# Kernel optimization log

Measured on AMD Instinct MI355X. Metric: run time of the kernel, lower is better.

Reference implementation:

```python
import jax, jax.numpy as jnp
import numpy as np

K = 7          # involution kernel size
PAD = (K - 1) // 2
C = 256        # channels
GC = 16        # group_channels (hardcoded in module)
G = C // GC    # groups = 16
RED = C // 4   # reduction channels = 64
EPS = 1e-5


def _bn_eval(x, gamma, beta, mean, var):
    # eval-mode BatchNorm2d over channel dim of NCHW
    inv = gamma / jnp.sqrt(var + EPS)
    return x * inv[None, :, None, None] + (beta - mean * inv)[None, :, None, None]


def setup_inputs() -> dict:
    key = jax.random.key(0)
    ks = jax.random.split(key, 12)
    x = jax.random.normal(ks[0], (8, C, 56, 56), dtype=jnp.float32)
    # conv1: 1x1, C -> C/4, no bias (followed by BN+ReLU)
    w1 = jax.random.normal(ks[1], (RED, C), dtype=jnp.float32) * (1.0 / np.sqrt(C))
    bn1_gamma = 1.0 + 0.1 * jax.random.normal(ks[2], (RED,), dtype=jnp.float32)
    bn1_beta = 0.1 * jax.random.normal(ks[3], (RED,), dtype=jnp.float32)
    bn1_mean = 0.1 * jax.random.normal(ks[4], (RED,), dtype=jnp.float32)
    bn1_var = jax.random.uniform(ks[5], (RED,), dtype=jnp.float32, minval=0.5, maxval=1.5)
    # conv2: 1x1, C/4 -> K^2 * groups, with bias, no BN/act
    w2 = jax.random.normal(ks[6], (K * K * G, RED), dtype=jnp.float32) * (1.0 / np.sqrt(RED))
    b2 = 0.1 * jax.random.normal(ks[7], (K * K * G,), dtype=jnp.float32)
    # final BN on output channels
    bn2_gamma = 1.0 + 0.1 * jax.random.normal(ks[8], (C,), dtype=jnp.float32)
    bn2_beta = 0.1 * jax.random.normal(ks[9], (C,), dtype=jnp.float32)
    bn2_mean = 0.1 * jax.random.normal(ks[10], (C,), dtype=jnp.float32)
    bn2_var = jax.random.uniform(ks[11], (C,), dtype=jnp.float32, minval=0.5, maxval=1.5)
    return {
        "x": x, "w1": w1,
        "bn1_gamma": bn1_gamma, "bn1_beta": bn1_beta, "bn1_mean": bn1_mean, "bn1_var": bn1_var,
        "w2": w2, "b2": b2,
        "bn2_gamma": bn2_gamma, "bn2_beta": bn2_beta, "bn2_mean": bn2_mean, "bn2_var": bn2_var,
    }


def reference(x, w1, bn1_gamma, bn1_beta, bn1_mean, bn1_var,
              w2, b2, bn2_gamma, bn2_beta, bn2_mean, bn2_var):
    b, c, h, w = x.shape
    # --- kernel generation branch (stride == 1, no avgpool) ---
    t = jnp.einsum('bchw,oc->bohw', x, w1)            # [b, RED, h, w]
    t = jax.nn.relu(_bn_eval(t, bn1_gamma, bn1_beta, bn1_mean, bn1_var))
    wgt = jnp.einsum('bchw,oc->bohw', t, w2) + b2[None, :, None, None]  # [b, K^2*G, h, w]
    wgt = wgt.reshape(b, G, K * K, h, w)
    # --- unfold: patches ordered (c, kh, kw) to match nn.Unfold ---
    xp = jnp.pad(x, ((0, 0), (0, 0), (PAD, PAD), (PAD, PAD)))
    patches = jnp.stack(
        [xp[:, :, i:i + h, j:j + w] for i in range(K) for j in range(K)],
        axis=2,
    )  # [b, c, K^2, h, w]
    patches = patches.reshape(b, G, GC, K * K, h, w)
    # --- per-pixel multiply-sum over kernel footprint ---
    out = jnp.einsum('bgkhw,bgckhw->bgchw', wgt, patches).reshape(b, c, h, w)
    out = jax.nn.relu(_bn_eval(out, bn2_gamma, bn2_beta, bn2_mean, bn2_var))
    return out
```

## Files before the change

kernel.cpp:

```cpp
#include <hip/hip_runtime.h>
#include <hip/hip_fp16.h>

#define NB   8
#define NC   256
#define HW   56
#define NPX  3136
#define RED  64
#define NG   16
#define GC   16
#define KS   7
#define KK   49
#define PADK 3
#define XPH  62
#define XPW  64
#define XPSLICE (XPH * XPW)
#define XT_RS 72
#define XT_CS 584
#define WSTR  68

typedef float f32x4 __attribute__((ext_vector_type(4)));
typedef _Float16 h16x4 __attribute__((ext_vector_type(4)));
typedef _Float16 h16x8 __attribute__((ext_vector_type(8)));

__global__ __launch_bounds__(256) void prep_kernel(
    const float* __restrict__ x, const float* __restrict__ w1,
    const float* __restrict__ w2, _Float16* __restrict__ xpad,
    _Float16* __restrict__ w1h, _Float16* __restrict__ w2h) {
    int bid = blockIdx.x;
    if (bid < NB * NC) {
        const float* xs = x + (size_t)bid * NPX;
        _Float16* xd = xpad + (size_t)bid * XPSLICE;
#pragma unroll 4
        for (int e = threadIdx.x; e < XPSLICE; e += 256) {
            int row = e >> 6, col = e & 63;
            int h = row - PADK, w = col - PADK;
            float v = (h >= 0 && h < HW && w >= 0 && w < HW) ? xs[h * HW + w] : 0.0f;
            xd[e] = (_Float16)v;
        }
    } else if (bid < NB * NC + NG) {
        int g = bid - NB * NC;
#pragma unroll 4
        for (int e = threadIdx.x; e < 4096; e += 256) {
            int m = e >> 6, k = e & 63;
            float v = (m < KK) ? w2[((size_t)g * KK + m) * RED + k] : 0.0f;
            w2h[(size_t)g * 4096 + e] = (_Float16)v;
        }
    } else {
#pragma unroll 4
        for (int e = threadIdx.x; e < 64 * 256; e += 256)
            w1h[e] = (_Float16)w1[e];
    }
}

__global__ __launch_bounds__(64) void conv1_kernel(
    const _Float16* __restrict__ xpad, const _Float16* __restrict__ w1h,
    const float* __restrict__ g1, const float* __restrict__ be1,
    const float* __restrict__ mu1, const float* __restrict__ var1,
    _Float16* __restrict__ tT) {
    int lane = threadIdx.x;
    int l15 = lane & 15, l4 = lane >> 4;
    int wgid = blockIdx.x;
    int b  = wgid & 7;
    int nt = wgid >> 3;
    int px = nt * 16 + l15;
    int h = px / HW, w = px % HW;

    const _Float16* xp = xpad + (size_t)b * NC * XPSLICE
                       + (h + PADK) * XPW + (w + PADK);

    f32x4 acc0 = {0,0,0,0}, acc1 = {0,0,0,0}, acc2 = {0,0,0,0}, acc3 = {0,0,0,0};
#pragma unroll
    for (int kk = 0; kk < 8; ++kk) {
        h16x8 bfr;
#pragma unroll
        for (int i = 0; i < 8; ++i)
            bfr[i] = xp[(size_t)(kk * 32 + l4 * 8 + i) * XPSLICE];
#pragma unroll
        for (int mt = 0; mt < 4; ++mt) {
            const _Float16* ap = w1h + (mt * 16 + l15) * NC + kk * 32 + l4 * 8;
            h16x8 a = *(const h16x8*)ap;
            f32x4 c = (mt == 0) ? acc0 : (mt == 1) ? acc1 : (mt == 2) ? acc2 : acc3;
            c = __builtin_amdgcn_mfma_f32_16x16x32_f16(a, bfr, c, 0, 0, 0);
            if (mt == 0) acc0 = c; else if (mt == 1) acc1 = c;
            else if (mt == 2) acc2 = c; else acc3 = c;
        }
    }

    _Float16* tb = tT + ((size_t)b * NPX + px) * RED;
#pragma unroll
    for (int mt = 0; mt < 4; ++mt) {
        f32x4 a = (mt == 0) ? acc0 : (mt == 1) ? acc1 : (mt == 2) ? acc2 : acc3;
        int o0 = mt * 16 + l4 * 4;
        h16x4 pk;
#pragma unroll
        for (int r = 0; r < 4; ++r) {
            int o = o0 + r;
            float inv = g1[o] * rsqrtf(var1[o] + 1e-5f);
            float v = a[r] * inv + (be1[o] - mu1[o] * inv);
            pk[r] = (_Float16)fmaxf(v, 0.0f);
        }
        *(h16x4*)(tb + o0) = pk;
    }
}

__global__ __launch_bounds__(256, 5) void involution_kernel(
    const _Float16* __restrict__ xpad, const _Float16* __restrict__ tT,
    const _Float16* __restrict__ w2h, const float* __restrict__ b2,
    const float* __restrict__ g2, const float* __restrict__ be2,
    const float* __restrict__ mu2, const float* __restrict__ var2,
    float* __restrict__ out) {
    __shared__ __align__(16) _Float16 xtap[GC * XT_CS];
    __shared__ __align__(16) _Float16 wls[KK * WSTR];

    int tid  = threadIdx.x;
    int lane = tid & 63;
    int wv   = __builtin_amdgcn_readfirstlane(tid >> 6);
    int wgid = blockIdx.x;
    int swz  = (wgid & 7) * 784 + (wgid >> 3);
    int tile = swz % 49;
    int g    = (swz / 49) & 15;
    int b    = swz / 784;
    int px0 = tile * 64;
    int h0  = px0 / HW;

    const _Float16* xpg = xpad + ((size_t)b * NC + (size_t)g * GC) * XPSLICE;

    h16x8 xr[4];
#pragma unroll
    for (int u = 0; u < 4; ++u) {
        int cid = u * 256 + tid;
        int ch  = cid >> 6;
        int rem = cid & 63;
        int rr  = rem >> 3, c8 = rem & 7;
        xr[u] = *(const h16x8*)(xpg + (size_t)ch * XPSLICE + (h0 + rr) * XPW + c8 * 8);
    }

    {
        int l15 = lane & 15, l4 = lane >> 4;
        int pxc = px0 + wv * 16 + l15;
        const _Float16* tp = tT + ((size_t)b * NPX + pxc) * RED + l4 * 8;
        h16x8 bfr0 = *(const h16x8*)tp;
        h16x8 bfr1 = *(const h16x8*)(tp + 32);

        const _Float16* wA = w2h + (size_t)g * 4096;
        const float* bg = b2 + (size_t)g * KK;
        f32x4 acc0 = {0,0,0,0}, acc1 = {0,0,0,0}, acc2 = {0,0,0,0}, acc3 = {0,0,0,0};
#pragma unroll
        for (int mt = 0; mt < 4; ++mt) {
            const _Float16* ap = wA + (mt * 16 + l15) * 64 + l4 * 8;
            h16x8 a0 = *(const h16x8*)(ap);
            h16x8 a1 = *(const h16x8*)(ap + 32);
            f32x4 a = (mt == 0) ? acc0 : (mt == 1) ? acc1 : (mt == 2) ? acc2 : acc3;
            a = __builtin_amdgcn_mfma_f32_16x16x32_f16(a0, bfr0, a, 0, 0, 0);
            a = __builtin_amdgcn_mfma_f32_16x16x32_f16(a1, bfr1, a, 0, 0, 0);
            if (mt == 0) acc0 = a; else if (mt == 1) acc1 = a;
            else if (mt == 2) acc2 = a; else acc3 = a;
        }
        _Float16* wl = wls + wv * 16 + l15;
#pragma unroll
        for (int mt = 0; mt < 4; ++mt) {
            f32x4 a = (mt == 0) ? acc0 : (mt == 1) ? acc1 : (mt == 2) ? acc2 : acc3;
#pragma unroll
            for (int r = 0; r < 4; ++r) {
                int k = mt * 16 + l4 * 4 + r;
                if (k < KK) wl[k * WSTR] = (_Float16)(a[r] + bg[k]);
            }
        }
    }

#pragma unroll
    for (int u = 0; u < 4; ++u) {
        int cid = u * 256 + tid;
        int ch  = cid >> 6;
        int rem = cid & 63;
        int rr  = rem >> 3, c8 = rem & 7;
        *(h16x8*)&xtap[ch * XT_CS + rr * XT_RS + c8 * 8] = xr[u];
    }
    __syncthreads();

    int quad = tid & 15;
    int ch   = tid >> 4;
    int pxl  = quad * 4;
    int px_a = px0 + pxl;
    int lh   = px_a / HW - h0;
    int w0   = px_a % HW;

    const _Float16* xr0 = xtap + ch * XT_CS + lh * XT_RS + w0;
    float acc0 = 0.f, acc1 = 0.f, acc2 = 0.f, acc3 = 0.f;
#pragma unroll
    for (int i = 0; i < KS; ++i) {
        h16x4 t0 = *(const h16x4*)(xr0 + i * XT_RS);
        h16x4 t1 = *(const h16x4*)(xr0 + i * XT_RS + 4);
        h16x4 t2 = *(const h16x4*)(xr0 + i * XT_RS + 8);
        float cc[12];
        cc[0] = (float)t0[0]; cc[1]  = (float)t0[1]; cc[2]  = (float)t0[2]; cc[3]  = (float)t0[3];
        cc[4] = (float)t1[0]; cc[5]  = (float)t1[1]; cc[6]  = (float)t1[2]; cc[7]  = (float)t1[3];
        cc[8] = (float)t2[0]; cc[9]  = (float)t2[1]; cc[10] = (float)t2[2]; cc[11] = (float)t2[3];
#pragma unroll
        for (int j = 0; j < KS; ++j) {
            h16x4 wp = *(const h16x4*)&wls[(i * KS + j) * WSTR + pxl];
            acc0 = fmaf((float)wp[0], cc[j + 0], acc0);
            acc1 = fmaf((float)wp[1], cc[j + 1], acc1);
            acc2 = fmaf((float)wp[2], cc[j + 2], acc2);
            acc3 = fmaf((float)wp[3], cc[j + 3], acc3);
        }
    }

    int c_ = g * GC + ch;
    float inv = g2[c_] * rsqrtf(var2[c_] + 1e-5f);
    float off = be2[c_] - mu2[c_] * inv;
    f32x4 o;
    o[0] = fmaxf(acc0 * inv + off, 0.0f);
    o[1] = fmaxf(acc1 * inv + off, 0.0f);
    o[2] = fmaxf(acc2 * inv + off, 0.0f);
    o[3] = fmaxf(acc3 * inv + off, 0.0f);
    *(f32x4*)(out + ((size_t)b * NC + c_) * NPX + px_a) = o;
}

extern "C" void kernel_launch(void* const* d_in, const int* in_sizes, int n_in,
                              void* d_out, int out_size, void* d_ws, size_t ws_size,
                              hipStream_t stream) {
    const float* x    = (const float*)d_in[0];
    const float* w1   = (const float*)d_in[1];
    const float* g1   = (const float*)d_in[2];
    const float* be1  = (const float*)d_in[3];
    const float* mu1  = (const float*)d_in[4];
    const float* var1 = (const float*)d_in[5];
    const float* w2   = (const float*)d_in[6];
    const float* b2   = (const float*)d_in[7];
    const float* g2   = (const float*)d_in[8];
    const float* be2  = (const float*)d_in[9];
    const float* mu2  = (const float*)d_in[10];
    const float* var2 = (const float*)d_in[11];
    float* outp = (float*)d_out;

    _Float16* xpad = (_Float16*)d_ws;
    char* p = (char*)d_ws + (size_t)NB * NC * XPSLICE * sizeof(_Float16);
    _Float16* tT = (_Float16*)p;
    p += (size_t)NB * NPX * RED * sizeof(_Float16);
    _Float16* w2h = (_Float16*)p;
    p += (size_t)NG * 4096 * sizeof(_Float16);
    _Float16* w1h = (_Float16*)p;

    prep_kernel<<<NB * NC + NG + 1, 256, 0, stream>>>(x, w1, w2, xpad, w1h, w2h);
    conv1_kernel<<<1568, 64, 0, stream>>>(xpad, w1h, g1, be1, mu1, var1, tT);
    involution_kernel<<<6272, 256, 0, stream>>>(
        xpad, tT, w2h, b2, g2, be2, mu2, var2, outp);
}
```

Before: 64.70 us.

## Add pixel-major fp16 copy of x so conv1 reads contiguous channel vectors

```diff
diff --git a/kernel.cpp b/kernel.cpp
--- a/kernel.cpp
+++ b/kernel.cpp
@@ -25,85 +25,104 @@
 __global__ __launch_bounds__(256) void prep_kernel(
     const float* __restrict__ x, const float* __restrict__ w1,
     const float* __restrict__ w2, _Float16* __restrict__ xpad,
-    _Float16* __restrict__ w1h, _Float16* __restrict__ w2h) {
+    _Float16* __restrict__ xT, _Float16* __restrict__ w1h,
+    _Float16* __restrict__ w2h) {
     int bid = blockIdx.x;
-    if (bid < NB * NC) {
-        const float* xs = x + (size_t)bid * NPX;
-        _Float16* xd = xpad + (size_t)bid * XPSLICE;
-#pragma unroll 4
-        for (int e = threadIdx.x; e < XPSLICE; e += 256) {
-            int row = e >> 6, col = e & 63;
-            int h = row - PADK, w = col - PADK;
-            float v = (h >= 0 && h < HW && w >= 0 && w < HW) ? xs[h * HW + w] : 0.0f;
-            xd[e] = (_Float16)v;
-        }
-    } else if (bid < NB * NC + NG) {
-        int g = bid - NB * NC;
+    if (bid < 392) {
+        __shared__ _Float16 tls[64][65];
+        int b = bid & 7, tile = bid >> 3;
+        int px0 = tile * 64;
+        int lane = threadIdx.x & 63;
+        int cq = threadIdx.x >> 6;
+        int px = px0 + lane;
+        int h = px / HW, w = px % HW;
+        const float* xb = x + (size_t)b * NC * NPX;
+#pragma unroll 1
+        for (int pass = 0; pass < 4; ++pass) {
+#pragma unroll
+            for (int rd = 0; rd < 16; ++rd) {
+                int c = pass * 64 + rd * 4 + cq;
+                _Float16 hv = (_Float16)xb[(size_t)c * NPX + px];
+                xpad[((size_t)b * NC + c) * XPSLICE + (h + PADK) * XPW + (w + PADK)] = hv;
+                tls[rd * 4 + cq][lane] = hv;
+            }
+            __syncthreads();
+#pragma unroll
+            for (int rd = 0; rd < 16; ++rd) {
+                int pxw = rd * 4 + cq;
+                xT[((size_t)b * NPX + px0 + pxw) * NC + pass * 64 + lane] =
+                    tls[lane][pxw];
+            }
+            __syncthreads();
+        }
+    } else if (bid < 408) {
+        int g = bid - 392;
 #pragma unroll 4
         for (int e = threadIdx.x; e < 4096; e += 256) {
             int m = e >> 6, k = e & 63;
             float v = (m < KK) ? w2[((size_t)g * KK + m) * RED + k] : 0.0f;
             w2h[(size_t)g * 4096 + e] = (_Float16)v;
         }
-    } else {
+    } else if (bid == 408) {
 #pragma unroll 4
         for (int e = threadIdx.x; e < 64 * 256; e += 256)
             w1h[e] = (_Float16)w1[e];
-    }
-}
-
-__global__ __launch_bounds__(64) void conv1_kernel(
-    const _Float16* __restrict__ xpad, const _Float16* __restrict__ w1h,
+    } else {
+        int blk = bid - 409;
+        int b = blk & 7;
+        int c0 = (blk >> 3) * 8;
+#pragma unroll 1
+        for (int si = 0; si < 8; ++si) {
+            _Float16* xd = xpad + ((size_t)b * NC + c0 + si) * XPSLICE;
+            for (int e = threadIdx.x; e < 832; e += 256) {
+                int row, col;
+                if (e < 192)      { row = e >> 6;              col = e & 63; }
+                else if (e < 384) { int f = e - 192; row = 59 + (f >> 6); col = f & 63; }
+                else              { int f = e - 384; row = 3 + (f >> 3);
+                                    int c8 = f & 7;  col = (c8 < 3) ? c8 : 56 + c8; }
+                xd[row * XPW + col] = (_Float16)0.0f;
+            }
+        }
+    }
+}
+
+__global__ __launch_bounds__(256) void conv1_kernel(
+    const _Float16* __restrict__ xT, const _Float16* __restrict__ w1h,
     const float* __restrict__ g1, const float* __restrict__ be1,
     const float* __restrict__ mu1, const float* __restrict__ var1,
     _Float16* __restrict__ tT) {
-    int lane = threadIdx.x;
-    int l15 = lane & 15, l4 = lane >> 4;
+    int lane = threadIdx.x & 63;
+    int wv   = __builtin_amdgcn_readfirstlane(threadIdx.x >> 6);
     int wgid = blockIdx.x;
     int b  = wgid & 7;
     int nt = wgid >> 3;
+    int l15 = lane & 15, l4 = lane >> 4;
     int px = nt * 16 + l15;
-    int h = px / HW, w = px % HW;
-
-    const _Float16* xp = xpad + (size_t)b * NC * XPSLICE
-                       + (h + PADK) * XPW + (w + PADK);
-
-    f32x4 acc0 = {0,0,0,0}, acc1 = {0,0,0,0}, acc2 = {0,0,0,0}, acc3 = {0,0,0,0};
+
+    const _Float16* bp = xT + ((size_t)b * NPX + px) * NC + l4 * 8;
+    const _Float16* ap = w1h + (wv * 16 + l15) * NC + l4 * 8;
+
+    f32x4 acc = {0, 0, 0, 0};
 #pragma unroll
     for (int kk = 0; kk < 8; ++kk) {
-        h16x8 bfr;
-#pragma unroll
-        for (int i = 0; i < 8; ++i)
-            bfr[i] = xp[(size_t)(kk * 32 + l4 * 8 + i) * XPSLICE];
-#pragma unroll
-        for (int mt = 0; mt < 4; ++mt) {
-            const _Float16* ap = w1h + (mt * 16 + l15) * NC + kk * 32 + l4 * 8;
-            h16x8 a = *(const h16x8*)ap;
-            f32x4 c = (mt == 0) ? acc0 : (mt == 1) ? acc1 : (mt == 2) ? acc2 : acc3;
-            c = __builtin_amdgcn_mfma_f32_16x16x32_f16(a, bfr, c, 0, 0, 0);
-            if (mt == 0) acc0 = c; else if (mt == 1) acc1 = c;
-            else if (mt == 2) acc2 = c; else acc3 = c;
-        }
-    }
-
-    _Float16* tb = tT + ((size_t)b * NPX + px) * RED;
-#pragma unroll
-    for (int mt = 0; mt < 4; ++mt) {
-        f32x4 a = (mt == 0) ? acc0 : (mt == 1) ? acc1 : (mt == 2) ? acc2 : acc3;
-        int o0 = mt * 16 + l4 * 4;
-        h16x4 pk;
-#pragma unroll
-        for (int r = 0; r < 4; ++r) {
-            int o = o0 + r;
-            float inv = g1[o] * rsqrtf(var1[o] + 1e-5f);
-            float v = a[r] * inv + (be1[o] - mu1[o] * inv);
-            pk[r] = (_Float16)fmaxf(v, 0.0f);
-        }
-        *(h16x4*)(tb + o0) = pk;
-    }
-}
-
-__global__ __launch_bounds__(256, 5) void involution_kernel(
+        h16x8 bfr = *(const h16x8*)(bp + kk * 32);
+        h16x8 a   = *(const h16x8*)(ap + kk * 32);
+        acc = __builtin_amdgcn_mfma_f32_16x16x32_f16(a, bfr, acc, 0, 0, 0);
+    }
+
+    int o0 = wv * 16 + l4 * 4;
+    h16x4 pk;
+#pragma unroll
+    for (int r = 0; r < 4; ++r) {
+        int o = o0 + r;
+        float inv = g1[o] * rsqrtf(var1[o] + 1e-5f);
+        float v = acc[r] * inv + (be1[o] - mu1[o] * inv);
+        pk[r] = (_Float16)fmaxf(v, 0.0f);
+    }
+    *(h16x4*)(tT + ((size_t)b * NPX + px) * RED + o0) = pk;
+}
+
+__global__ __launch_bounds__(256, 6) void involution_kernel(
     const _Float16* __restrict__ xpad, const _Float16* __restrict__ tT,
     const _Float16* __restrict__ w2h, const float* __restrict__ b2,
     const float* __restrict__ g2, const float* __restrict__ be2,
@@ -235,15 +254,13 @@
     float* outp = (float*)d_out;
 
     _Float16* xpad = (_Float16*)d_ws;
-    char* p = (char*)d_ws + (size_t)NB * NC * XPSLICE * sizeof(_Float16);
-    _Float16* tT = (_Float16*)p;
-    p += (size_t)NB * NPX * RED * sizeof(_Float16);
-    _Float16* w2h = (_Float16*)p;
-    p += (size_t)NG * 4096 * sizeof(_Float16);
-    _Float16* w1h = (_Float16*)p;
-
-    prep_kernel<<<NB * NC + NG + 1, 256, 0, stream>>>(x, w1, w2, xpad, w1h, w2h);
-    conv1_kernel<<<1568, 64, 0, stream>>>(xpad, w1h, g1, be1, mu1, var1, tT);
+    _Float16* xT   = xpad + (size_t)NB * NC * XPSLICE;
+    _Float16* tT   = xT + (size_t)NB * NPX * NC;
+    _Float16* w2h  = tT + (size_t)NB * NPX * RED;
+    _Float16* w1h  = w2h + (size_t)NG * 4096;
+
+    prep_kernel<<<665, 256, 0, stream>>>(x, w1, w2, xpad, xT, w1h, w2h);
+    conv1_kernel<<<1568, 256, 0, stream>>>(xT, w1h, g1, be1, mu1, var1, tT);
     involution_kernel<<<6272, 256, 0, stream>>>(
         xpad, tT, w2h, b2, g2, be2, mu2, var2, outp);
 }
```

After: 71.92 us. 11.2% more time.

## Enlarge involution tile to 4 rows per block with 8 pixels per thread

Applied to the files above, without the earlier changes.

```diff
diff --git a/kernel.cpp b/kernel.cpp
--- a/kernel.cpp
+++ b/kernel.cpp
@@ -14,9 +14,10 @@
 #define XPH  62
 #define XPW  64
 #define XPSLICE (XPH * XPW)
-#define XT_RS 72
-#define XT_CS 584
-#define WSTR  68
+#define TPX  224
+#define NT2  14
+#define XT2_CS 644
+#define WSTR2  232
 
 typedef float f32x4 __attribute__((ext_vector_type(4)));
 typedef _Float16 h16x4 __attribute__((ext_vector_type(4)));
@@ -103,118 +104,137 @@
     }
 }
 
-__global__ __launch_bounds__(256, 5) void involution_kernel(
+__global__ __launch_bounds__(448, 3) void involution_kernel(
     const _Float16* __restrict__ xpad, const _Float16* __restrict__ tT,
     const _Float16* __restrict__ w2h, const float* __restrict__ b2,
     const float* __restrict__ g2, const float* __restrict__ be2,
     const float* __restrict__ mu2, const float* __restrict__ var2,
     float* __restrict__ out) {
-    __shared__ __align__(16) _Float16 xtap[GC * XT_CS];
-    __shared__ __align__(16) _Float16 wls[KK * WSTR];
+    __shared__ __align__(16) _Float16 xtap[GC * XT2_CS];
+    __shared__ __align__(16) _Float16 wls[KK * WSTR2];
 
     int tid  = threadIdx.x;
     int lane = tid & 63;
     int wv   = __builtin_amdgcn_readfirstlane(tid >> 6);
     int wgid = blockIdx.x;
-    int swz  = (wgid & 7) * 784 + (wgid >> 3);
-    int tile = swz % 49;
-    int g    = (swz / 49) & 15;
-    int b    = swz / 784;
-    int px0 = tile * 64;
-    int h0  = px0 / HW;
+    int swz  = (wgid & 7) * 224 + (wgid >> 3);
+    int b    = swz / 224;
+    int rem  = swz % 224;
+    int g    = rem / NT2;
+    int tile = rem % NT2;
+    int px0 = tile * TPX;
+    int R0  = tile * 4;
 
     const _Float16* xpg = xpad + ((size_t)b * NC + (size_t)g * GC) * XPSLICE;
 
-    h16x8 xr[4];
-#pragma unroll
-    for (int u = 0; u < 4; ++u) {
-        int cid = u * 256 + tid;
-        int ch  = cid >> 6;
-        int rem = cid & 63;
-        int rr  = rem >> 3, c8 = rem & 7;
-        xr[u] = *(const h16x8*)(xpg + (size_t)ch * XPSLICE + (h0 + rr) * XPW + c8 * 8);
+    h16x8 xr[3];
+#pragma unroll
+    for (int u = 0; u < 3; ++u) {
+        int cid = u * 448 + tid;
+        if (cid < 1280) {
+            int ch = cid / 80;
+            int rm = cid % 80;
+            int rr = rm >> 3, c8 = rm & 7;
+            xr[u] = *(const h16x8*)(xpg + (size_t)ch * XPSLICE
+                                    + (R0 + rr) * XPW + c8 * 8);
+        }
     }
 
     {
         int l15 = lane & 15, l4 = lane >> 4;
-        int pxc = px0 + wv * 16 + l15;
-        const _Float16* tp = tT + ((size_t)b * NPX + pxc) * RED + l4 * 8;
-        h16x8 bfr0 = *(const h16x8*)tp;
-        h16x8 bfr1 = *(const h16x8*)(tp + 32);
-
         const _Float16* wA = w2h + (size_t)g * 4096;
         const float* bg = b2 + (size_t)g * KK;
-        f32x4 acc0 = {0,0,0,0}, acc1 = {0,0,0,0}, acc2 = {0,0,0,0}, acc3 = {0,0,0,0};
+        h16x8 a0[4], a1[4];
 #pragma unroll
         for (int mt = 0; mt < 4; ++mt) {
             const _Float16* ap = wA + (mt * 16 + l15) * 64 + l4 * 8;
-            h16x8 a0 = *(const h16x8*)(ap);
-            h16x8 a1 = *(const h16x8*)(ap + 32);
-            f32x4 a = (mt == 0) ? acc0 : (mt == 1) ? acc1 : (mt == 2) ? acc2 : acc3;
-            a = __builtin_amdgcn_mfma_f32_16x16x32_f16(a0, bfr0, a, 0, 0, 0);
-            a = __builtin_amdgcn_mfma_f32_16x16x32_f16(a1, bfr1, a, 0, 0, 0);
-            if (mt == 0) acc0 = a; else if (mt == 1) acc1 = a;
-            else if (mt == 2) acc2 = a; else acc3 = a;
-        }
-        _Float16* wl = wls + wv * 16 + l15;
-#pragma unroll
-        for (int mt = 0; mt < 4; ++mt) {
-            f32x4 a = (mt == 0) ? acc0 : (mt == 1) ? acc1 : (mt == 2) ? acc2 : acc3;
-#pragma unroll
-            for (int r = 0; r < 4; ++r) {
-                int k = mt * 16 + l4 * 4 + r;
-                if (k < KK) wl[k * WSTR] = (_Float16)(a[r] + bg[k]);
+            a0[mt] = *(const h16x8*)(ap);
+            a1[mt] = *(const h16x8*)(ap + 32);
+        }
+#pragma unroll
+        for (int it = 0; it < 2; ++it) {
+            int nt = wv * 2 + it;
+            int pxc = px0 + nt * 16 + l15;
+            const _Float16* tp = tT + ((size_t)b * NPX + pxc) * RED + l4 * 8;
+            h16x8 bfr0 = *(const h16x8*)tp;
+            h16x8 bfr1 = *(const h16x8*)(tp + 32);
+
+            f32x4 acc0 = {0,0,0,0}, acc1 = {0,0,0,0},
+                  acc2 = {0,0,0,0}, acc3 = {0,0,0,0};
+#pragma unroll
+            for (int mt = 0; mt < 4; ++mt) {
+                f32x4 a = (mt == 0) ? acc0 : (mt == 1) ? acc1
+                        : (mt == 2) ? acc2 : acc3;
+                a = __builtin_amdgcn_mfma_f32_16x16x32_f16(a0[mt], bfr0, a, 0, 0, 0);
+                a = __builtin_amdgcn_mfma_f32_16x16x32_f16(a1[mt], bfr1, a, 0, 0, 0);
+                if (mt == 0) acc0 = a; else if (mt == 1) acc1 = a;
+                else if (mt == 2) acc2 = a; else acc3 = a;
             }
-        }
-    }
-
-#pragma unroll
-    for (int u = 0; u < 4; ++u) {
-        int cid = u * 256 + tid;
-        int ch  = cid >> 6;
-        int rem = cid & 63;
-        int rr  = rem >> 3, c8 = rem & 7;
-        *(h16x8*)&xtap[ch * XT_CS + rr * XT_RS + c8 * 8] = xr[u];
+            _Float16* wl = wls + nt * 16 + l15;
+#pragma unroll
+            for (int mt = 0; mt < 4; ++mt) {
+                f32x4 a = (mt == 0) ? acc0 : (mt == 1) ? acc1
+                        : (mt == 2) ? acc2 : acc3;
+#pragma unroll
+                for (int r = 0; r < 4; ++r) {
+                    int k = mt * 16 + l4 * 4 + r;
+                    if (k < KK) wl[k * WSTR2] = (_Float16)(a[r] + bg[k]);
+                }
+            }
+        }
+    }
+
+#pragma unroll
+    for (int u = 0; u < 3; ++u) {
+        int cid = u * 448 + tid;
+        if (cid < 1280) {
+            int ch = cid / 80;
+            int rm = cid % 80;
+            int rr = rm >> 3, c8 = rm & 7;
+            *(h16x8*)&xtap[ch * XT2_CS + rr * 64 + c8 * 8] = xr[u];
+        }
     }
     __syncthreads();
 
-    int quad = tid & 15;
-    int ch   = tid >> 4;
-    int pxl  = quad * 4;
-    int px_a = px0 + pxl;
-    int lh   = px_a / HW - h0;
-    int w0   = px_a % HW;
-
-    const _Float16* xr0 = xtap + ch * XT_CS + lh * XT_RS + w0;
-    float acc0 = 0.f, acc1 = 0.f, acc2 = 0.f, acc3 = 0.f;
+    int octet = tid >> 4;
+    int ch    = tid & 15;
+    int lin   = octet * 8;
+    int lh    = lin / 56;
+    int w0    = lin % 56;
+
+    const _Float16* xb0 = xtap + ch * XT2_CS + lh * 64 + w0;
+    float acc[8];
+#pragma unroll
+    for (int p = 0; p < 8; ++p) acc[p] = 0.0f;
+
 #pragma unroll
     for (int i = 0; i < KS; ++i) {
-        h16x4 t0 = *(const h16x4*)(xr0 + i * XT_RS);
-        h16x4 t1 = *(const h16x4*)(xr0 + i * XT_RS + 4);
-        h16x4 t2 = *(const h16x4*)(xr0 + i * XT_RS + 8);
-        float cc[12];
-        cc[0] = (float)t0[0]; cc[1]  = (float)t0[1]; cc[2]  = (float)t0[2]; cc[3]  = (float)t0[3];
-        cc[4] = (float)t1[0]; cc[5]  = (float)t1[1]; cc[6]  = (float)t1[2]; cc[7]  = (float)t1[3];
-        cc[8] = (float)t2[0]; cc[9]  = (float)t2[1]; cc[10] = (float)t2[2]; cc[11] = (float)t2[3];
+        h16x8 t0 = *(const h16x8*)(xb0 + i * 64);
+        h16x8 t1 = *(const h16x8*)(xb0 + i * 64 + 8);
+        float cc[16];
+#pragma unroll
+        for (int p = 0; p < 8; ++p) { cc[p] = (float)t0[p]; cc[8 + p] = (float)t1[p]; }
 #pragma unroll
         for (int j = 0; j < KS; ++j) {
-            h16x4 wp = *(const h16x4*)&wls[(i * KS + j) * WSTR + pxl];
-            acc0 = fmaf((float)wp[0], cc[j + 0], acc0);
-            acc1 = fmaf((float)wp[1], cc[j + 1], acc1);
-            acc2 = fmaf((float)wp[2], cc[j + 2], acc2);
-            acc3 = fmaf((float)wp[3], cc[j + 3], acc3);
+            h16x8 wq = *(const h16x8*)&wls[(i * KS + j) * WSTR2 + lin];
+#pragma unroll
+            for (int p = 0; p < 8; ++p)
+                acc[p] = fmaf((float)wq[p], cc[j + p], acc[p]);
         }
     }
 
     int c_ = g * GC + ch;
     float inv = g2[c_] * rsqrtf(var2[c_] + 1e-5f);
     float off = be2[c_] - mu2[c_] * inv;
-    f32x4 o;
-    o[0] = fmaxf(acc0 * inv + off, 0.0f);
-    o[1] = fmaxf(acc1 * inv + off, 0.0f);
-    o[2] = fmaxf(acc2 * inv + off, 0.0f);
-    o[3] = fmaxf(acc3 * inv + off, 0.0f);
-    *(f32x4*)(out + ((size_t)b * NC + c_) * NPX + px_a) = o;
+    float* op = out + ((size_t)b * NC + c_) * NPX + px0 + lin;
+    f32x4 o0, o1;
+#pragma unroll
+    for (int p = 0; p < 4; ++p) {
+        o0[p] = fmaxf(acc[p] * inv + off, 0.0f);
+        o1[p] = fmaxf(acc[4 + p] * inv + off, 0.0f);
+    }
+    *(f32x4*)(op)     = o0;
+    *(f32x4*)(op + 4) = o1;
 }
 
 extern "C" void kernel_launch(void* const* d_in, const int* in_sizes, int n_in,
@@ -235,15 +255,12 @@
     float* outp = (float*)d_out;
 
     _Float16* xpad = (_Float16*)d_ws;
-    char* p = (char*)d_ws + (size_t)NB * NC * XPSLICE * sizeof(_Float16);
-    _Float16* tT = (_Float16*)p;
-    p += (size_t)NB * NPX * RED * sizeof(_Float16);
-    _Float16* w2h = (_Float16*)p;
-    p += (size_t)NG * 4096 * sizeof(_Float16);
-    _Float16* w1h = (_Float16*)p;
+    _Float16* tT   = xpad + (size_t)NB * NC * XPSLICE;
+    _Float16* w2h  = tT + (size_t)NB * NPX * RED;
+    _Float16* w1h  = w2h + (size_t)NG * 4096;
 
     prep_kernel<<<NB * NC + NG + 1, 256, 0, stream>>>(x, w1, w2, xpad, w1h, w2h);
     conv1_kernel<<<1568, 64, 0, stream>>>(xpad, w1h, g1, be1, mu1, var1, tT);
-    involution_kernel<<<6272, 256, 0, stream>>>(
+    involution_kernel<<<1792, 448, 0, stream>>>(
         xpad, tT, w2h, b2, g2, be2, mu2, var2, outp);
 }
```

After: 64.14 us. No clear change (-0.9%).

## Make involution blocks persistent over four tiles with register double-buffered prefetch

Applied to the files above, without the earlier changes.

```diff
diff --git a/kernel.cpp b/kernel.cpp
--- a/kernel.cpp
+++ b/kernel.cpp
@@ -103,10 +103,10 @@
     }
 }
 
-__global__ __launch_bounds__(256, 5) void involution_kernel(
+__global__ __launch_bounds__(256) void involution_kernel(
     const _Float16* __restrict__ xpad, const _Float16* __restrict__ tT,
     const _Float16* __restrict__ w2h, const float* __restrict__ b2,
-    const float* __restrict__ g2, const float* __restrict__ be2,
+    const float* __restrict__ g2v, const float* __restrict__ be2,
     const float* __restrict__ mu2, const float* __restrict__ var2,
     float* __restrict__ out) {
     __shared__ __align__(16) _Float16 xtap[GC * XT_CS];
@@ -115,106 +115,142 @@
     int tid  = threadIdx.x;
     int lane = tid & 63;
     int wv   = __builtin_amdgcn_readfirstlane(tid >> 6);
-    int wgid = blockIdx.x;
-    int swz  = (wgid & 7) * 784 + (wgid >> 3);
-    int tile = swz % 49;
-    int g    = (swz / 49) & 15;
-    int b    = swz / 784;
-    int px0 = tile * 64;
-    int h0  = px0 / HW;
-
-    const _Float16* xpg = xpad + ((size_t)b * NC + (size_t)g * GC) * XPSLICE;
-
-    h16x8 xr[4];
-#pragma unroll
-    for (int u = 0; u < 4; ++u) {
-        int cid = u * 256 + tid;
-        int ch  = cid >> 6;
-        int rem = cid & 63;
-        int rr  = rem >> 3, c8 = rem & 7;
-        xr[u] = *(const h16x8*)(xpg + (size_t)ch * XPSLICE + (h0 + rr) * XPW + c8 * 8);
-    }
+    int l15 = lane & 15, l4 = lane >> 4;
+    int quad = tid & 15;
+    int chB  = tid >> 4;
+    int bid = blockIdx.x;
+    int b   = bid & 7;
+    int idx = bid >> 3;
+
+    h16x8 xrP[2][4];
+    h16x8 bfP[2][2];
 
     {
-        int l15 = lane & 15, l4 = lane >> 4;
+        int un = idx * 4;
+        int g = un / 49, tile = un % 49;
+        int px0 = tile * 64, h0 = px0 / HW;
+        const _Float16* xpg = xpad + ((size_t)b * NC + (size_t)g * GC) * XPSLICE;
+#pragma unroll
+        for (int su = 0; su < 4; ++su) {
+            int c_ = su * 256 + tid;
+            int ch = c_ >> 6, rem = c_ & 63, rr = rem >> 3, c8 = rem & 7;
+            xrP[0][su] = *(const h16x8*)(xpg + (size_t)ch * XPSLICE
+                                         + (h0 + rr) * XPW + c8 * 8);
+        }
         int pxc = px0 + wv * 16 + l15;
         const _Float16* tp = tT + ((size_t)b * NPX + pxc) * RED + l4 * 8;
-        h16x8 bfr0 = *(const h16x8*)tp;
-        h16x8 bfr1 = *(const h16x8*)(tp + 32);
-
-        const _Float16* wA = w2h + (size_t)g * 4096;
-        const float* bg = b2 + (size_t)g * KK;
-        f32x4 acc0 = {0,0,0,0}, acc1 = {0,0,0,0}, acc2 = {0,0,0,0}, acc3 = {0,0,0,0};
-#pragma unroll
-        for (int mt = 0; mt < 4; ++mt) {
-            const _Float16* ap = wA + (mt * 16 + l15) * 64 + l4 * 8;
-            h16x8 a0 = *(const h16x8*)(ap);
-            h16x8 a1 = *(const h16x8*)(ap + 32);
-            f32x4 a = (mt == 0) ? acc0 : (mt == 1) ? acc1 : (mt == 2) ? acc2 : acc3;
-            a = __builtin_amdgcn_mfma_f32_16x16x32_f16(a0, bfr0, a, 0, 0, 0);
-            a = __builtin_amdgcn_mfma_f32_16x16x32_f16(a1, bfr1, a, 0, 0, 0);
-            if (mt == 0) acc0 = a; else if (mt == 1) acc1 = a;
-            else if (mt == 2) acc2 = a; else acc3 = a;
-        }
-        _Float16* wl = wls + wv * 16 + l15;
-#pragma unroll
-        for (int mt = 0; mt < 4; ++mt) {
-            f32x4 a = (mt == 0) ? acc0 : (mt == 1) ? acc1 : (mt == 2) ? acc2 : acc3;
-#pragma unroll
-            for (int r = 0; r < 4; ++r) {
-                int k = mt * 16 + l4 * 4 + r;
-                if (k < KK) wl[k * WSTR] = (_Float16)(a[r] + bg[k]);
-            }
-        }
+        bfP[0][0] = *(const h16x8*)tp;
+        bfP[0][1] = *(const h16x8*)(tp + 32);
     }
 
 #pragma unroll
     for (int u = 0; u < 4; ++u) {
-        int cid = u * 256 + tid;
-        int ch  = cid >> 6;
-        int rem = cid & 63;
-        int rr  = rem >> 3, c8 = rem & 7;
-        *(h16x8*)&xtap[ch * XT_CS + rr * XT_RS + c8 * 8] = xr[u];
-    }
-    __syncthreads();
-
-    int quad = tid & 15;
-    int ch   = tid >> 4;
-    int pxl  = quad * 4;
-    int px_a = px0 + pxl;
-    int lh   = px_a / HW - h0;
-    int w0   = px_a % HW;
-
-    const _Float16* xr0 = xtap + ch * XT_CS + lh * XT_RS + w0;
-    float acc0 = 0.f, acc1 = 0.f, acc2 = 0.f, acc3 = 0.f;
-#pragma unroll
-    for (int i = 0; i < KS; ++i) {
-        h16x4 t0 = *(const h16x4*)(xr0 + i * XT_RS);
-        h16x4 t1 = *(const h16x4*)(xr0 + i * XT_RS + 4);
-        h16x4 t2 = *(const h16x4*)(xr0 + i * XT_RS + 8);
-        float cc[12];
-        cc[0] = (float)t0[0]; cc[1]  = (float)t0[1]; cc[2]  = (float)t0[2]; cc[3]  = (float)t0[3];
-        cc[4] = (float)t1[0]; cc[5]  = (float)t1[1]; cc[6]  = (float)t1[2]; cc[7]  = (float)t1[3];
-        cc[8] = (float)t2[0]; cc[9]  = (float)t2[1]; cc[10] = (float)t2[2]; cc[11] = (float)t2[3];
-#pragma unroll
-        for (int j = 0; j < KS; ++j) {
-            h16x4 wp = *(const h16x4*)&wls[(i * KS + j) * WSTR + pxl];
-            acc0 = fmaf((float)wp[0], cc[j + 0], acc0);
-            acc1 = fmaf((float)wp[1], cc[j + 1], acc1);
-            acc2 = fmaf((float)wp[2], cc[j + 2], acc2);
-            acc3 = fmaf((float)wp[3], cc[j + 3], acc3);
-        }
-    }
-
-    int c_ = g * GC + ch;
-    float inv = g2[c_] * rsqrtf(var2[c_] + 1e-5f);
-    float off = be2[c_] - mu2[c_] * inv;
-    f32x4 o;
-    o[0] = fmaxf(acc0 * inv + off, 0.0f);
-    o[1] = fmaxf(acc1 * inv + off, 0.0f);
-    o[2] = fmaxf(acc2 * inv + off, 0.0f);
-    o[3] = fmaxf(acc3 * inv + off, 0.0f);
-    *(f32x4*)(out + ((size_t)b * NC + c_) * NPX + px_a) = o;
+        const int cur = u & 1;
+        const int nxt = cur ^ 1;
+        int un = idx * 4 + u;
+        int g = un / 49, tile = un % 49;
+        int px0 = tile * 64, h0 = px0 / HW;
+
+        asm volatile("s_waitcnt lgkmcnt(0)" ::: "memory");
+        __builtin_amdgcn_s_barrier();
+        __builtin_amdgcn_sched_barrier(0);
+
+#pragma unroll
+        for (int su = 0; su < 4; ++su) {
+            int c_ = su * 256 + tid;
+            int ch = c_ >> 6, rem = c_ & 63, rr = rem >> 3, c8 = rem & 7;
+            *(h16x8*)&xtap[ch * XT_CS + rr * XT_RS + c8 * 8] = xrP[cur][su];
+        }
+
+        {
+            const _Float16* wA = w2h + (size_t)g * 4096;
+            const float* bg = b2 + (size_t)g * KK;
+            f32x4 acc0 = {0,0,0,0}, acc1 = {0,0,0,0},
+                  acc2 = {0,0,0,0}, acc3 = {0,0,0,0};
+#pragma unroll
+            for (int mt = 0; mt < 4; ++mt) {
+                const _Float16* ap = wA + (mt * 16 + l15) * 64 + l4 * 8;
+                h16x8 a0 = *(const h16x8*)(ap);
+                h16x8 a1 = *(const h16x8*)(ap + 32);
+                f32x4 a = (mt == 0) ? acc0 : (mt == 1) ? acc1
+                        : (mt == 2) ? acc2 : acc3;
+                a = __builtin_amdgcn_mfma_f32_16x16x32_f16(a0, bfP[cur][0], a, 0, 0, 0);
+                a = __builtin_amdgcn_mfma_f32_16x16x32_f16(a1, bfP[cur][1], a, 0, 0, 0);
+                if (mt == 0) acc0 = a; else if (mt == 1) acc1 = a;
+                else if (mt == 2) acc2 = a; else acc3 = a;
+            }
+            _Float16* wl = wls + wv * 16 + l15;
+#pragma unroll
+            for (int mt = 0; mt < 4; ++mt) {
+                f32x4 a = (mt == 0) ? acc0 : (mt == 1) ? acc1
+                        : (mt == 2) ? acc2 : acc3;
+#pragma unroll
+                for (int r = 0; r < 4; ++r) {
+                    int k = mt * 16 + l4 * 4 + r;
+                    if (k < KK) wl[k * WSTR] = (_Float16)(a[r] + bg[k]);
+                }
+            }
+        }
+
+        int c_out = g * GC + chB;
+        float inv = g2v[c_out] * rsqrtf(var2[c_out] + 1e-5f);
+        float off = be2[c_out] - mu2[c_out] * inv;
+
+        if (u < 3) {
+            int un2 = un + 1;
+            int gN = un2 / 49, tileN = un2 % 49;
+            int px0N = tileN * 64, h0N = px0N / HW;
+            const _Float16* xpgN = xpad + ((size_t)b * NC + (size_t)gN * GC) * XPSLICE;
+#pragma unroll
+            for (int su = 0; su < 4; ++su) {
+                int c_ = su * 256 + tid;
+                int ch = c_ >> 6, rem = c_ & 63, rr = rem >> 3, c8 = rem & 7;
+                xrP[nxt][su] = *(const h16x8*)(xpgN + (size_t)ch * XPSLICE
+                                               + (h0N + rr) * XPW + c8 * 8);
+            }
+            int pxcN = px0N + wv * 16 + l15;
+            const _Float16* tpN = tT + ((size_t)b * NPX + pxcN) * RED + l4 * 8;
+            bfP[nxt][0] = *(const h16x8*)tpN;
+            bfP[nxt][1] = *(const h16x8*)(tpN + 32);
+        }
+
+        asm volatile("s_waitcnt lgkmcnt(0)" ::: "memory");
+        __builtin_amdgcn_s_barrier();
+        __builtin_amdgcn_sched_barrier(0);
+
+        int pxl  = quad * 4;
+        int px_a = px0 + pxl;
+        int lh   = px_a / HW - h0;
+        int w0   = px_a % HW;
+
+        const _Float16* xr0 = xtap + chB * XT_CS + lh * XT_RS + w0;
+        float a0 = 0.f, a1 = 0.f, a2 = 0.f, a3 = 0.f;
+#pragma unroll
+        for (int i = 0; i < KS; ++i) {
+            h16x4 t0 = *(const h16x4*)(xr0 + i * XT_RS);
+            h16x4 t1 = *(const h16x4*)(xr0 + i * XT_RS + 4);
+            h16x4 t2 = *(const h16x4*)(xr0 + i * XT_RS + 8);
+            float cc[12];
+            cc[0] = (float)t0[0]; cc[1]  = (float)t0[1]; cc[2]  = (float)t0[2]; cc[3]  = (float)t0[3];
+            cc[4] = (float)t1[0]; cc[5]  = (float)t1[1]; cc[6]  = (float)t1[2]; cc[7]  = (float)t1[3];
+            cc[8] = (float)t2[0]; cc[9]  = (float)t2[1]; cc[10] = (float)t2[2]; cc[11] = (float)t2[3];
+#pragma unroll
+            for (int j = 0; j < KS; ++j) {
+                h16x4 wp = *(const h16x4*)&wls[(i * KS + j) * WSTR + pxl];
+                a0 = fmaf((float)wp[0], cc[j + 0], a0);
+                a1 = fmaf((float)wp[1], cc[j + 1], a1);
+                a2 = fmaf((float)wp[2], cc[j + 2], a2);
+                a3 = fmaf((float)wp[3], cc[j + 3], a3);
+            }
+        }
+
+        f32x4 o;
+        o[0] = fmaxf(a0 * inv + off, 0.0f);
+        o[1] = fmaxf(a1 * inv + off, 0.0f);
+        o[2] = fmaxf(a2 * inv + off, 0.0f);
+        o[3] = fmaxf(a3 * inv + off, 0.0f);
+        *(f32x4*)(out + ((size_t)b * NC + c_out) * NPX + px_a) = o;
+    }
 }
 
 extern "C" void kernel_launch(void* const* d_in, const int* in_sizes, int n_in,
@@ -235,15 +271,12 @@
     float* outp = (float*)d_out;
 
     _Float16* xpad = (_Float16*)d_ws;
-    char* p = (char*)d_ws + (size_t)NB * NC * XPSLICE * sizeof(_Float16);
-    _Float16* tT = (_Float16*)p;
-    p += (size_t)NB * NPX * RED * sizeof(_Float16);
-    _Float16* w2h = (_Float16*)p;
-    p += (size_t)NG * 4096 * sizeof(_Float16);
-    _Float16* w1h = (_Float16*)p;
+    _Float16* tT   = xpad + (size_t)NB * NC * XPSLICE;
+    _Float16* w2h  = tT + (size_t)NB * NPX * RED;
+    _Float16* w1h  = w2h + (size_t)NG * 4096;
 
     prep_kernel<<<NB * NC + NG + 1, 256, 0, stream>>>(x, w1, w2, xpad, w1h, w2h);
     conv1_kernel<<<1568, 64, 0, stream>>>(xpad, w1h, g1, be1, mu1, var1, tT);
-    involution_kernel<<<6272, 256, 0, stream>>>(
+    involution_kernel<<<1568, 256, 0, stream>>>(
         xpad, tT, w2h, b2, g2, be2, mu2, var2, outp);
 }
```

Result: slower. 75.08 us (+16.1%).
